# Kernel optimization log

Hardware: AMD Instinct MI355X
Metric: run time of the kernel (lower is better)

The kernel has to match this reference:

```python
import jax, jax.numpy as jnp
import numpy as np

DIMS = 512
B, H, W = 16, 64, 64
C8, C2 = DIMS // 8, DIMS // 2


def _maxpool2(x):
    # 2x2 max pool, stride 2. x: [B, C, H, W] -> [B, C, H//2, W//2]
    b, c, h, w = x.shape
    return x.reshape(b, c, h // 2, 2, w // 2, 2).max(axis=(3, 5))


def _conv1x1(x, w, b):
    # 1x1 conv == channel matmul. x: [B, C_in, H, W], w: [C_out, C_in], b: [C_out]
    return jnp.einsum('oc,bchw->bohw', w, x) + b[None, :, None, None]


def setup_inputs() -> dict:
    key = jax.random.key(0)
    ks = jax.random.split(key, 10)
    s_in = 1.0 / np.sqrt(DIMS)
    s_c2 = 1.0 / np.sqrt(C2)
    return {
        'inputs':  jax.random.normal(ks[0], (B, DIMS, H, W), jnp.float32),
        'w_theta': jax.random.normal(ks[1], (C8, DIMS), jnp.float32) * s_in,
        'b_theta': jax.random.normal(ks[2], (C8,), jnp.float32) * 0.01,
        'w_phi':   jax.random.normal(ks[3], (C8, DIMS), jnp.float32) * s_in,
        'b_phi':   jax.random.normal(ks[4], (C8,), jnp.float32) * 0.01,
        'w_g':     jax.random.normal(ks[5], (C2, DIMS), jnp.float32) * s_in,
        'b_g':     jax.random.normal(ks[6], (C2,), jnp.float32) * 0.01,
        'w_attn':  jax.random.normal(ks[7], (DIMS, C2), jnp.float32) * s_c2,
        'b_attn':  jax.random.normal(ks[8], (DIMS,), jnp.float32) * 0.01,
        'sigma':   jnp.full((1,), 0.5, jnp.float32),
    }


def reference(inputs, w_theta, b_theta, w_phi, b_phi, w_g, b_g, w_attn, b_attn, sigma):
    b, c, h, w = inputs.shape
    hw, hw4 = h * w, (h * w) // 4

    # theta: [B, HW, C//8]
    theta = _conv1x1(inputs, w_theta, b_theta).reshape(b, c // 8, hw).transpose(0, 2, 1)
    # phi: maxpooled keys [B, C//8, HW/4]
    phi = _maxpool2(_conv1x1(inputs, w_phi, b_phi)).reshape(b, c // 8, hw4)
    # attention over downsampled positions
    attn = jax.nn.softmax(jnp.einsum('bnc,bcm->bnm', theta, phi), axis=-1)
    # g: maxpooled values [B, HW/4, C//2]
    g = _maxpool2(_conv1x1(inputs, w_g, b_g)).reshape(b, c // 2, hw4).transpose(0, 2, 1)
    # attend, back to image layout [B, C//2, H, W]
    attn_g = jnp.einsum('bnm,bmc->bnc', attn, g).transpose(0, 2, 1).reshape(b, c // 2, h, w)
    attn_g = _conv1x1(attn_g, w_attn, b_attn)
    return inputs + sigma * attn_g
```

## Files before the change

kernel.cpp:

```cpp
#include <hip/hip_runtime.h>
#include <cstdint>
#include <cstddef>


typedef float f32x4 __attribute__((ext_vector_type(4)));
typedef short bf16x8 __attribute__((ext_vector_type(8)));

static __device__ __forceinline__ float max4f(float a, float b, float c, float d) {
  return fmaxf(fmaxf(a, b), fmaxf(c, d));
}

static __device__ __forceinline__ unsigned short f2bf(float f) {
  unsigned int u = __float_as_uint(f);
  unsigned int r = u + 0x7fffu + ((u >> 16) & 1u);
  return (unsigned short)(r >> 16);
}

__global__ __launch_bounds__(256) void pack_kernel(
    const float* __restrict__ wt, const float* __restrict__ bt,
    const float* __restrict__ wp, const float* __restrict__ bp,
    const float* __restrict__ wg, const float* __restrict__ bg,
    const float* __restrict__ wa,
    unsigned short* __restrict__ Wcat_bf, float* __restrict__ bcat,
    unsigned short* __restrict__ Wa_bf) {
  int i = blockIdx.x * 256 + threadIdx.x;
  if (i < 384 * 512) {
    int o = i >> 9, k = i & 511;
    float v;
    if (o < 64)       v = wt[o * 512 + k];
    else if (o < 128) v = wp[(o - 64) * 512 + k];
    else              v = wg[(o - 128) * 512 + k];
    Wcat_bf[i] = f2bf(v);
  }
  if (i < 512 * 256) Wa_bf[i] = f2bf(wa[i]);
  if (i < 384) {
    float v;
    if (i < 64)       v = bt[i];
    else if (i < 128) v = bp[i - 64];
    else              v = bg[i - 128];
    bcat[i] = v;
  }
}

__global__ __launch_bounds__(256) void transpose_kernel(
    const float* __restrict__ X, unsigned short* __restrict__ Xbf_T) {
  __shared__ unsigned short smT[64 * 516];
  const int b = blockIdx.y, n0 = blockIdx.x * 64;
  const int t = threadIdx.x;
  const float* Xb = X + (size_t)b * 512 * 4096;

  {
    const int nq = t & 15, kr = t >> 4;
#pragma unroll 4
    for (int it = 0; it < 32; ++it) {
      int k = it * 16 + kr;
      float4 v = *(const float4*)&Xb[(size_t)k * 4096 + n0 + nq * 4];
      smT[(nq * 4 + 0) * 516 + k] = f2bf(v.x);
      smT[(nq * 4 + 1) * 516 + k] = f2bf(v.y);
      smT[(nq * 4 + 2) * 516 + k] = f2bf(v.z);
      smT[(nq * 4 + 3) * 516 + k] = f2bf(v.w);
    }
  }
  __syncthreads();

  {
    const int c = t & 63, w = t >> 6;
#pragma unroll 4
    for (int i = 0; i < 16; ++i) {
      int n = w + 4 * i;
      const unsigned short* src = &smT[n * 516 + c * 8];
      uint2 lo = *(const uint2*)&src[0];
      uint2 hi = *(const uint2*)&src[4];
      uint4 v; v.x = lo.x; v.y = lo.y; v.z = hi.x; v.w = hi.y;
      *(uint4*)&Xbf_T[((size_t)b * 4096 + n0 + n) * 512 + c * 8] = v;
    }
  }
}

__global__ __launch_bounds__(256, 3) void conv_pool_kernel(
    const unsigned short* __restrict__ Xbf_T, const unsigned short* __restrict__ Wcat_bf,
    const float* __restrict__ bcat,
    unsigned short* __restrict__ theta_t, unsigned short* __restrict__ phi_t,
    unsigned short* __restrict__ g_t) {
  const int b = blockIdx.z, mt = blockIdx.y, nt = blockIdx.x;
  const int n0 = nt * 128;
  __shared__ float cs[64][132];
  const int t = threadIdx.x;
  const int wave = t >> 6, lane = t & 63;
  const int wm = wave >> 1, wn = wave & 1;
  const int l16 = lane & 15, quad = lane >> 4;

  const unsigned short* aptr =
      Wcat_bf + (size_t)(mt * 128 + wm * 64 + l16) * 512 + quad * 8;
  const unsigned short* bptr =
      Xbf_T + ((size_t)b * 4096 + n0 + wn * 64 + l16) * 512 + quad * 8;

  f32x4 acc[4][4];
#pragma unroll
  for (int i = 0; i < 4; ++i)
#pragma unroll
    for (int j = 0; j < 4; ++j) acc[i][j] = (f32x4)(0.f);

  for (int k0 = 0; k0 < 512; k0 += 32) {
    bf16x8 af[4], bfr[4];
#pragma unroll
    for (int am = 0; am < 4; ++am) af[am] = *(const bf16x8*)(aptr + (size_t)am * 16 * 512 + k0);
#pragma unroll
    for (int bn = 0; bn < 4; ++bn) bfr[bn] = *(const bf16x8*)(bptr + (size_t)bn * 16 * 512 + k0);
#pragma unroll
    for (int am = 0; am < 4; ++am)
#pragma unroll
      for (int bn = 0; bn < 4; ++bn)
        acc[am][bn] = __builtin_amdgcn_mfma_f32_16x16x32_bf16(af[am], bfr[bn], acc[am][bn], 0, 0, 0);
  }

  for (int s = 0; s < 2; ++s) {
    const int m0 = mt * 128 + s * 64;
    const float bias_base = 0.f; (void)bias_base;
    if (wm == s) {
#pragma unroll
      for (int am = 0; am < 4; ++am)
#pragma unroll
        for (int bn = 0; bn < 4; ++bn)
#pragma unroll
          for (int reg = 0; reg < 4; ++reg)
            cs[am * 16 + quad * 4 + reg][wn * 64 + bn * 16 + l16] =
                acc[am][bn][reg] + bcat[m0 + am * 16 + quad * 4 + reg];
    }
    __syncthreads();
    if (m0 < 64) {
      int col = t >> 1, half = t & 1;
      unsigned short vals[32];
#pragma unroll
      for (int i = 0; i < 32; ++i) vals[i] = f2bf(cs[half * 32 + i][col]);
      unsigned short* dst = theta_t + ((size_t)b * 4096 + n0 + col) * 64 + half * 32;
#pragma unroll
      for (int j = 0; j < 4; ++j) ((uint4*)dst)[j] = ((const uint4*)vals)[j];
    } else if (m0 < 128) {
      int px = t >> 3, ch0 = (t & 7) * 8;
      unsigned short v[8];
#pragma unroll
      for (int j = 0; j < 8; ++j) {
        int ch = ch0 + j;
        v[j] = f2bf(max4f(cs[ch][2 * px], cs[ch][2 * px + 1],
                          cs[ch][64 + 2 * px], cs[ch][64 + 2 * px + 1]));
      }
      *(uint4*)&phi_t[((size_t)b * 1024 + nt * 32 + px) * 64 + ch0] = *(const uint4*)v;
    } else {
      int ch = t >> 2, px0 = (t & 3) * 8;
      int gc = m0 - 128 + ch;
      unsigned short v[8];
#pragma unroll
      for (int j = 0; j < 8; ++j) {
        int px = px0 + j;
        v[j] = f2bf(max4f(cs[ch][2 * px], cs[ch][2 * px + 1],
                          cs[ch][64 + 2 * px], cs[ch][64 + 2 * px + 1]));
      }
      *(uint4*)&g_t[((size_t)b * 256 + gc) * 1024 + nt * 32 + px0] = *(const uint4*)v;
    }
    __syncthreads();
  }
}

__global__ __launch_bounds__(256, 2) void attn_kernel(
    const unsigned short* __restrict__ theta, const unsigned short* __restrict__ phi,
    const unsigned short* __restrict__ g, unsigned short* __restrict__ Obf) {
  const int b = blockIdx.y, q0 = blockIdx.x * 32;
  __shared__ unsigned short S_s[32][1032];
  __shared__ float smax[4][32];
  __shared__ float ssum[4][32];
  const int t = threadIdx.x;
  const int w = t >> 6, lane = t & 63;
  const int l16 = lane & 15, quad = lane >> 4;
  const int m0w = w * 256;

  bf16x8 afrag[2][2];
#pragma unroll
  for (int qt = 0; qt < 2; ++qt)
#pragma unroll
    for (int kh = 0; kh < 2; ++kh)
      afrag[qt][kh] = *(const bf16x8*)&theta[((size_t)b * 4096 + q0 + qt * 16 + l16) * 64 +
                                             kh * 32 + quad * 8];

  f32x4 acc[2][16];
#pragma unroll
  for (int qt = 0; qt < 2; ++qt)
#pragma unroll
    for (int mt = 0; mt < 16; ++mt) acc[qt][mt] = (f32x4)(0.f);

  const unsigned short* phiB = phi + (size_t)b * 1024 * 64;
#pragma unroll
  for (int mt = 0; mt < 16; ++mt) {
    int m = m0w + mt * 16 + l16;
    bf16x8 b0 = *(const bf16x8*)&phiB[(size_t)m * 64 + quad * 8];
    bf16x8 b1 = *(const bf16x8*)&phiB[(size_t)m * 64 + 32 + quad * 8];
#pragma unroll
    for (int qt = 0; qt < 2; ++qt) {
      acc[qt][mt] = __builtin_amdgcn_mfma_f32_16x16x32_bf16(afrag[qt][0], b0, acc[qt][mt], 0, 0, 0);
      acc[qt][mt] = __builtin_amdgcn_mfma_f32_16x16x32_bf16(afrag[qt][1], b1, acc[qt][mt], 0, 0, 0);
    }
  }

  float mx8[8];
#pragma unroll
  for (int r = 0; r < 8; ++r) {
    int qt = r >> 2, reg = r & 3;
    float m = acc[qt][0][reg];
#pragma unroll
    for (int mt = 1; mt < 16; ++mt) m = fmaxf(m, acc[qt][mt][reg]);
#pragma unroll
    for (int d = 1; d < 16; d <<= 1) m = fmaxf(m, __shfl_xor(m, d));
    mx8[r] = m;
  }
  if (l16 == 0) {
#pragma unroll
    for (int r = 0; r < 8; ++r) smax[w][(r >> 2) * 16 + quad * 4 + (r & 3)] = mx8[r];
  }
  __syncthreads();
  float gmx[8];
#pragma unroll
  for (int r = 0; r < 8; ++r) {
    int q = (r >> 2) * 16 + quad * 4 + (r & 3);
    gmx[r] = fmaxf(fmaxf(smax[0][q], smax[1][q]), fmaxf(smax[2][q], smax[3][q]));
  }
  float sum8[8];
#pragma unroll
  for (int r = 0; r < 8; ++r) sum8[r] = 0.f;
#pragma unroll
  for (int qt = 0; qt < 2; ++qt)
#pragma unroll
    for (int mt = 0; mt < 16; ++mt)
#pragma unroll
      for (int reg = 0; reg < 4; ++reg) {
        int r = qt * 4 + reg;
        float p = __expf(acc[qt][mt][reg] - gmx[r]);
        acc[qt][mt][reg] = p;
        sum8[r] += p;
      }
#pragma unroll
  for (int r = 0; r < 8; ++r) {
#pragma unroll
    for (int d = 1; d < 16; d <<= 1) sum8[r] += __shfl_xor(sum8[r], d);
  }
  if (l16 == 0) {
#pragma unroll
    for (int r = 0; r < 8; ++r) ssum[w][(r >> 2) * 16 + quad * 4 + (r & 3)] = sum8[r];
  }
  __syncthreads();
  float inv8[8];
#pragma unroll
  for (int r = 0; r < 8; ++r) {
    int q = (r >> 2) * 16 + quad * 4 + (r & 3);
    inv8[r] = 1.0f / (ssum[0][q] + ssum[1][q] + ssum[2][q] + ssum[3][q]);
  }
#pragma unroll
  for (int qt = 0; qt < 2; ++qt)
#pragma unroll
    for (int mt = 0; mt < 16; ++mt)
#pragma unroll
      for (int reg = 0; reg < 4; ++reg) {
        int q = qt * 16 + quad * 4 + reg;
        S_s[q][m0w + mt * 16 + l16] = f2bf(acc[qt][mt][reg] * inv8[qt * 4 + reg]);
      }
  __syncthreads();

  const int cbase = w * 64;
  f32x4 accO[2][4];
#pragma unroll
  for (int qt = 0; qt < 2; ++qt)
#pragma unroll
    for (int ct = 0; ct < 4; ++ct) accO[qt][ct] = (f32x4)(0.f);
  const unsigned short* gB = g + (size_t)b * 256 * 1024;
  for (int k0 = 0; k0 < 1024; k0 += 32) {
    bf16x8 a0 = *(const bf16x8*)&S_s[l16][k0 + quad * 8];
    bf16x8 a1 = *(const bf16x8*)&S_s[16 + l16][k0 + quad * 8];
#pragma unroll
    for (int ct = 0; ct < 4; ++ct) {
      bf16x8 bb = *(const bf16x8*)&gB[(size_t)(cbase + ct * 16 + l16) * 1024 + k0 + quad * 8];
      accO[0][ct] = __builtin_amdgcn_mfma_f32_16x16x32_bf16(a0, bb, accO[0][ct], 0, 0, 0);
      accO[1][ct] = __builtin_amdgcn_mfma_f32_16x16x32_bf16(a1, bb, accO[1][ct], 0, 0, 0);
    }
  }
  unsigned short* Ob = Obf + ((size_t)b * 4096 + q0) * 256;
#pragma unroll
  for (int qt = 0; qt < 2; ++qt)
#pragma unroll
    for (int ct = 0; ct < 4; ++ct)
#pragma unroll
      for (int reg = 0; reg < 4; ++reg)
        Ob[(size_t)(qt * 16 + quad * 4 + reg) * 256 + cbase + ct * 16 + l16] =
            f2bf(accO[qt][ct][reg]);
}

__global__ __launch_bounds__(256, 3) void out_kernel(
    const float* __restrict__ X, const unsigned short* __restrict__ Obf,
    const unsigned short* __restrict__ Wa_bf, const float* __restrict__ ba,
    const float* __restrict__ sigma, float* __restrict__ out) {
  const int b = blockIdx.z, mt = blockIdx.y, nt = blockIdx.x;
  const int t = threadIdx.x;
  const int wave = t >> 6, lane = t & 63;
  const int wm = wave >> 1, wn = wave & 1;
  const int l16 = lane & 15, quad = lane >> 4;

  const unsigned short* aptr = Wa_bf + (size_t)(mt * 128 + wm * 64 + l16) * 256 + quad * 8;
  const unsigned short* bptr =
      Obf + ((size_t)b * 4096 + nt * 128 + wn * 64 + l16) * 256 + quad * 8;

  f32x4 acc[4][4];
#pragma unroll
  for (int i = 0; i < 4; ++i)
#pragma unroll
    for (int j = 0; j < 4; ++j) acc[i][j] = (f32x4)(0.f);

#pragma unroll
  for (int k0 = 0; k0 < 256; k0 += 32) {
    bf16x8 af[4], bfr[4];
#pragma unroll
    for (int am = 0; am < 4; ++am) af[am] = *(const bf16x8*)(aptr + (size_t)am * 16 * 256 + k0);
#pragma unroll
    for (int bn = 0; bn < 4; ++bn) bfr[bn] = *(const bf16x8*)(bptr + (size_t)bn * 16 * 256 + k0);
#pragma unroll
    for (int am = 0; am < 4; ++am)
#pragma unroll
      for (int bn = 0; bn < 4; ++bn)
        acc[am][bn] = __builtin_amdgcn_mfma_f32_16x16x32_bf16(af[am], bfr[bn], acc[am][bn], 0, 0, 0);
  }

  const float sg = sigma[0];
#pragma unroll
  for (int am = 0; am < 4; ++am) {
#pragma unroll
    for (int reg = 0; reg < 4; ++reg) {
      int m = mt * 128 + wm * 64 + am * 16 + quad * 4 + reg;
      float bias = ba[m];
      size_t rowoff = ((size_t)b * 512 + m) * 4096 + nt * 128 + wn * 64;
#pragma unroll
      for (int bn = 0; bn < 4; ++bn) {
        size_t idx = rowoff + bn * 16 + l16;
        out[idx] = X[idx] + sg * (acc[am][bn][reg] + bias);
      }
    }
  }
}

extern "C" void kernel_launch(void* const* d_in, const int* in_sizes, int n_in,
                              void* d_out, int out_size, void* d_ws, size_t ws_size,
                              hipStream_t stream) {
  (void)in_sizes; (void)n_in; (void)out_size; (void)ws_size;
  const float* X  = (const float*)d_in[0];
  const float* wt = (const float*)d_in[1];
  const float* bt = (const float*)d_in[2];
  const float* wp = (const float*)d_in[3];
  const float* bp = (const float*)d_in[4];
  const float* wg = (const float*)d_in[5];
  const float* bg = (const float*)d_in[6];
  const float* wa = (const float*)d_in[7];
  const float* ba = (const float*)d_in[8];
  const float* sg = (const float*)d_in[9];
  float* out = (float*)d_out;
  char* base = (char*)d_ws;

  unsigned short* Wcat_bf = (unsigned short*)(base);
  unsigned short* Wa_bf   = (unsigned short*)(base + 0x60000);
  float*          bcat    = (float*)(base + 0xA0000);
  unsigned short* theta_t = (unsigned short*)(base + (1u << 20));
  unsigned short* phi_t   = (unsigned short*)(base + (9u << 20));
  unsigned short* g_t     = (unsigned short*)(base + (11u << 20));
  unsigned short* Xbf_T   = (unsigned short*)(base + (19u << 20));
  unsigned short* Obf     = (unsigned short*)(base + (19u << 20));

  pack_kernel<<<dim3(768), dim3(256), 0, stream>>>(wt, bt, wp, bp, wg, bg, wa,
                                                   Wcat_bf, bcat, Wa_bf);
  transpose_kernel<<<dim3(64, 16), dim3(256), 0, stream>>>(X, Xbf_T);
  conv_pool_kernel<<<dim3(32, 3, 16), dim3(256), 0, stream>>>(Xbf_T, Wcat_bf, bcat,
                                                              theta_t, phi_t, g_t);
  attn_kernel<<<dim3(128, 16), dim3(256), 0, stream>>>(theta_t, phi_t, g_t, Obf);
  out_kernel<<<dim3(32, 4, 16), dim3(256), 0, stream>>>(X, Obf, Wa_bf, ba, sg, out);
}
```

Measured before the change: 607.2 us.

## Stage GEMM tiles via async global-to-LDS loads and widen attention to 8 waves

The conv_pool and out GEMM kernels now stage each 32-wide K slice of both operands into LDS with global_load_lds 16-byte async copies. The MFMA fragments are then read from LDS instead of being loaded directly from global memory by each wave, which aims to cut redundant global traffic and improve coalescing. The price is two barriers per K step and no double buffering, so load latency is not overlapped with compute. Separately, attn_kernel moves to 512 threads (8 waves), each wave covering half as many keys and output channels. Its softmax now combines per-wave max and sum statistics in one pass, removing a barrier.

Result: faster. 573.9 us (-5.5%).

```diff
diff --git a/kernel.cpp b/kernel.cpp
--- a/kernel.cpp
+++ b/kernel.cpp
@@ -14,6 +14,12 @@
   unsigned int u = __float_as_uint(f);
   unsigned int r = u + 0x7fffu + ((u >> 16) & 1u);
   return (unsigned short)(r >> 16);
+}
+
+static __device__ __forceinline__ void async_ld16(void* lds, const void* g) {
+  __builtin_amdgcn_global_load_lds(
+      (const __attribute__((address_space(1))) unsigned int*)g,
+      (__attribute__((address_space(3))) unsigned int*)lds, 16, 0, 0);
 }
 
 __global__ __launch_bounds__(256) void pack_kernel(
@@ -62,7 +68,6 @@
     }
   }
   __syncthreads();
-
   {
     const int c = t & 63, w = t >> 6;
 #pragma unroll 4
@@ -84,16 +89,19 @@
     unsigned short* __restrict__ g_t) {
   const int b = blockIdx.z, mt = blockIdx.y, nt = blockIdx.x;
   const int n0 = nt * 128;
-  __shared__ float cs[64][132];
+  __shared__ union {
+    struct { unsigned short A[128 * 32]; unsigned short B[128 * 32]; } st;
+    float cs[64][132];
+  } sm;
   const int t = threadIdx.x;
   const int wave = t >> 6, lane = t & 63;
   const int wm = wave >> 1, wn = wave & 1;
   const int l16 = lane & 15, quad = lane >> 4;
-
-  const unsigned short* aptr =
-      Wcat_bf + (size_t)(mt * 128 + wm * 64 + l16) * 512 + quad * 8;
-  const unsigned short* bptr =
-      Xbf_T + ((size_t)b * 4096 + n0 + wn * 64 + l16) * 512 + quad * 8;
+  const int srow = lane >> 2, skq = (lane & 3) * 8;
+
+  const unsigned short* gA = Wcat_bf + (size_t)(mt * 128) * 512 + skq;
+  const unsigned short* gB = Xbf_T + ((size_t)b * 4096 + n0) * 512 + skq;
+  const int r0 = wave * 32;
 
   f32x4 acc[4][4];
 #pragma unroll
@@ -101,22 +109,31 @@
 #pragma unroll
     for (int j = 0; j < 4; ++j) acc[i][j] = (f32x4)(0.f);
 
+  const int abase = (wm * 64 + l16) * 32 + quad * 8;
+  const int bbase = (wn * 64 + l16) * 32 + quad * 8;
+
   for (int k0 = 0; k0 < 512; k0 += 32) {
+    __syncthreads();
+    async_ld16(&sm.st.A[(r0) * 32],      gA + (size_t)(r0 + srow) * 512 + k0);
+    async_ld16(&sm.st.A[(r0 + 16) * 32], gA + (size_t)(r0 + 16 + srow) * 512 + k0);
+    async_ld16(&sm.st.B[(r0) * 32],      gB + (size_t)(r0 + srow) * 512 + k0);
+    async_ld16(&sm.st.B[(r0 + 16) * 32], gB + (size_t)(r0 + 16 + srow) * 512 + k0);
+    __syncthreads();
     bf16x8 af[4], bfr[4];
 #pragma unroll
-    for (int am = 0; am < 4; ++am) af[am] = *(const bf16x8*)(aptr + (size_t)am * 16 * 512 + k0);
-#pragma unroll
-    for (int bn = 0; bn < 4; ++bn) bfr[bn] = *(const bf16x8*)(bptr + (size_t)bn * 16 * 512 + k0);
+    for (int am = 0; am < 4; ++am) af[am] = *(const bf16x8*)&sm.st.A[abase + am * 16 * 32];
+#pragma unroll
+    for (int bn = 0; bn < 4; ++bn) bfr[bn] = *(const bf16x8*)&sm.st.B[bbase + bn * 16 * 32];
 #pragma unroll
     for (int am = 0; am < 4; ++am)
 #pragma unroll
       for (int bn = 0; bn < 4; ++bn)
         acc[am][bn] = __builtin_amdgcn_mfma_f32_16x16x32_bf16(af[am], bfr[bn], acc[am][bn], 0, 0, 0);
   }
+  __syncthreads();
 
   for (int s = 0; s < 2; ++s) {
     const int m0 = mt * 128 + s * 64;
-    const float bias_base = 0.f; (void)bias_base;
     if (wm == s) {
 #pragma unroll
       for (int am = 0; am < 4; ++am)
@@ -124,7 +141,7 @@
         for (int bn = 0; bn < 4; ++bn)
 #pragma unroll
           for (int reg = 0; reg < 4; ++reg)
-            cs[am * 16 + quad * 4 + reg][wn * 64 + bn * 16 + l16] =
+            sm.cs[am * 16 + quad * 4 + reg][wn * 64 + bn * 16 + l16] =
                 acc[am][bn][reg] + bcat[m0 + am * 16 + quad * 4 + reg];
     }
     __syncthreads();
@@ -132,7 +149,7 @@
       int col = t >> 1, half = t & 1;
       unsigned short vals[32];
 #pragma unroll
-      for (int i = 0; i < 32; ++i) vals[i] = f2bf(cs[half * 32 + i][col]);
+      for (int i = 0; i < 32; ++i) vals[i] = f2bf(sm.cs[half * 32 + i][col]);
       unsigned short* dst = theta_t + ((size_t)b * 4096 + n0 + col) * 64 + half * 32;
 #pragma unroll
       for (int j = 0; j < 4; ++j) ((uint4*)dst)[j] = ((const uint4*)vals)[j];
@@ -142,8 +159,8 @@
 #pragma unroll
       for (int j = 0; j < 8; ++j) {
         int ch = ch0 + j;
-        v[j] = f2bf(max4f(cs[ch][2 * px], cs[ch][2 * px + 1],
-                          cs[ch][64 + 2 * px], cs[ch][64 + 2 * px + 1]));
+        v[j] = f2bf(max4f(sm.cs[ch][2 * px], sm.cs[ch][2 * px + 1],
+                          sm.cs[ch][64 + 2 * px], sm.cs[ch][64 + 2 * px + 1]));
       }
       *(uint4*)&phi_t[((size_t)b * 1024 + nt * 32 + px) * 64 + ch0] = *(const uint4*)v;
     } else {
@@ -153,8 +170,8 @@
 #pragma unroll
       for (int j = 0; j < 8; ++j) {
         int px = px0 + j;
-        v[j] = f2bf(max4f(cs[ch][2 * px], cs[ch][2 * px + 1],
-                          cs[ch][64 + 2 * px], cs[ch][64 + 2 * px + 1]));
+        v[j] = f2bf(max4f(sm.cs[ch][2 * px], sm.cs[ch][2 * px + 1],
+                          sm.cs[ch][64 + 2 * px], sm.cs[ch][64 + 2 * px + 1]));
       }
       *(uint4*)&g_t[((size_t)b * 256 + gc) * 1024 + nt * 32 + px0] = *(const uint4*)v;
     }
@@ -162,17 +179,16 @@
   }
 }
 
-__global__ __launch_bounds__(256, 2) void attn_kernel(
+__global__ __launch_bounds__(512, 4) void attn_kernel(
     const unsigned short* __restrict__ theta, const unsigned short* __restrict__ phi,
     const unsigned short* __restrict__ g, unsigned short* __restrict__ Obf) {
   const int b = blockIdx.y, q0 = blockIdx.x * 32;
   __shared__ unsigned short S_s[32][1032];
-  __shared__ float smax[4][32];
-  __shared__ float ssum[4][32];
+  __shared__ float2 sstat[32][8];
   const int t = threadIdx.x;
   const int w = t >> 6, lane = t & 63;
   const int l16 = lane & 15, quad = lane >> 4;
-  const int m0w = w * 256;
+  const int m0w = w * 128;
 
   bf16x8 afrag[2][2];
 #pragma unroll
@@ -182,15 +198,15 @@
       afrag[qt][kh] = *(const bf16x8*)&theta[((size_t)b * 4096 + q0 + qt * 16 + l16) * 64 +
                                              kh * 32 + quad * 8];
 
-  f32x4 acc[2][16];
-#pragma unroll
-  for (int qt = 0; qt < 2; ++qt)
-#pragma unroll
-    for (int mt = 0; mt < 16; ++mt) acc[qt][mt] = (f32x4)(0.f);
+  f32x4 acc[2][8];
+#pragma unroll
+  for (int qt = 0; qt < 2; ++qt)
+#pragma unroll
+    for (int mt = 0; mt < 8; ++mt) acc[qt][mt] = (f32x4)(0.f);
 
   const unsigned short* phiB = phi + (size_t)b * 1024 * 64;
 #pragma unroll
-  for (int mt = 0; mt < 16; ++mt) {
+  for (int mt = 0; mt < 8; ++mt) {
     int m = m0w + mt * 16 + l16;
     bf16x8 b0 = *(const bf16x8*)&phiB[(size_t)m * 64 + quad * 8];
     bf16x8 b1 = *(const bf16x8*)&phiB[(size_t)m * 64 + 32 + quad * 8];
@@ -201,39 +217,26 @@
     }
   }
 
-  float mx8[8];
+  float mx8[8], sum8[8];
 #pragma unroll
   for (int r = 0; r < 8; ++r) {
     int qt = r >> 2, reg = r & 3;
     float m = acc[qt][0][reg];
 #pragma unroll
-    for (int mt = 1; mt < 16; ++mt) m = fmaxf(m, acc[qt][mt][reg]);
+    for (int mt = 1; mt < 8; ++mt) m = fmaxf(m, acc[qt][mt][reg]);
 #pragma unroll
     for (int d = 1; d < 16; d <<= 1) m = fmaxf(m, __shfl_xor(m, d));
     mx8[r] = m;
-  }
-  if (l16 == 0) {
-#pragma unroll
-    for (int r = 0; r < 8; ++r) smax[w][(r >> 2) * 16 + quad * 4 + (r & 3)] = mx8[r];
-  }
-  __syncthreads();
-  float gmx[8];
-#pragma unroll
-  for (int r = 0; r < 8; ++r) {
-    int q = (r >> 2) * 16 + quad * 4 + (r & 3);
-    gmx[r] = fmaxf(fmaxf(smax[0][q], smax[1][q]), fmaxf(smax[2][q], smax[3][q]));
-  }
-  float sum8[8];
-#pragma unroll
-  for (int r = 0; r < 8; ++r) sum8[r] = 0.f;
-#pragma unroll
-  for (int qt = 0; qt < 2; ++qt)
-#pragma unroll
-    for (int mt = 0; mt < 16; ++mt)
+    sum8[r] = 0.f;
+  }
+#pragma unroll
+  for (int qt = 0; qt < 2; ++qt)
+#pragma unroll
+    for (int mt = 0; mt < 8; ++mt)
 #pragma unroll
       for (int reg = 0; reg < 4; ++reg) {
         int r = qt * 4 + reg;
-        float p = __expf(acc[qt][mt][reg] - gmx[r]);
+        float p = __expf(acc[qt][mt][reg] - mx8[r]);
         acc[qt][mt][reg] = p;
         sum8[r] += p;
       }
@@ -244,38 +247,51 @@
   }
   if (l16 == 0) {
 #pragma unroll
-    for (int r = 0; r < 8; ++r) ssum[w][(r >> 2) * 16 + quad * 4 + (r & 3)] = sum8[r];
+    for (int r = 0; r < 8; ++r) {
+      int q = (r >> 2) * 16 + quad * 4 + (r & 3);
+      sstat[q][w] = make_float2(mx8[r], sum8[r]);
+    }
   }
   __syncthreads();
-  float inv8[8];
+
+  float alpha[8];
 #pragma unroll
   for (int r = 0; r < 8; ++r) {
     int q = (r >> 2) * 16 + quad * 4 + (r & 3);
-    inv8[r] = 1.0f / (ssum[0][q] + ssum[1][q] + ssum[2][q] + ssum[3][q]);
-  }
-#pragma unroll
-  for (int qt = 0; qt < 2; ++qt)
-#pragma unroll
-    for (int mt = 0; mt < 16; ++mt)
+    float2 st[8];
+#pragma unroll
+    for (int j = 0; j < 4; ++j) ((float4*)st)[j] = *(const float4*)&sstat[q][j * 2];
+    float mg = st[0].x;
+#pragma unroll
+    for (int j = 1; j < 8; ++j) mg = fmaxf(mg, st[j].x);
+    float sg = 0.f;
+#pragma unroll
+    for (int j = 0; j < 8; ++j) sg += st[j].y * __expf(st[j].x - mg);
+    alpha[r] = __expf(mx8[r] - mg) / sg;
+  }
+#pragma unroll
+  for (int qt = 0; qt < 2; ++qt)
+#pragma unroll
+    for (int mt = 0; mt < 8; ++mt)
 #pragma unroll
       for (int reg = 0; reg < 4; ++reg) {
         int q = qt * 16 + quad * 4 + reg;
-        S_s[q][m0w + mt * 16 + l16] = f2bf(acc[qt][mt][reg] * inv8[qt * 4 + reg]);
+        S_s[q][m0w + mt * 16 + l16] = f2bf(acc[qt][mt][reg] * alpha[qt * 4 + reg]);
       }
   __syncthreads();
 
-  const int cbase = w * 64;
-  f32x4 accO[2][4];
-#pragma unroll
-  for (int qt = 0; qt < 2; ++qt)
-#pragma unroll
-    for (int ct = 0; ct < 4; ++ct) accO[qt][ct] = (f32x4)(0.f);
+  const int cbase = w * 32;
+  f32x4 accO[2][2];
+#pragma unroll
+  for (int qt = 0; qt < 2; ++qt)
+#pragma unroll
+    for (int ct = 0; ct < 2; ++ct) accO[qt][ct] = (f32x4)(0.f);
   const unsigned short* gB = g + (size_t)b * 256 * 1024;
   for (int k0 = 0; k0 < 1024; k0 += 32) {
     bf16x8 a0 = *(const bf16x8*)&S_s[l16][k0 + quad * 8];
     bf16x8 a1 = *(const bf16x8*)&S_s[16 + l16][k0 + quad * 8];
 #pragma unroll
-    for (int ct = 0; ct < 4; ++ct) {
+    for (int ct = 0; ct < 2; ++ct) {
       bf16x8 bb = *(const bf16x8*)&gB[(size_t)(cbase + ct * 16 + l16) * 1024 + k0 + quad * 8];
       accO[0][ct] = __builtin_amdgcn_mfma_f32_16x16x32_bf16(a0, bb, accO[0][ct], 0, 0, 0);
       accO[1][ct] = __builtin_amdgcn_mfma_f32_16x16x32_bf16(a1, bb, accO[1][ct], 0, 0, 0);
@@ -285,7 +301,7 @@
 #pragma unroll
   for (int qt = 0; qt < 2; ++qt)
 #pragma unroll
-    for (int ct = 0; ct < 4; ++ct)
+    for (int ct = 0; ct < 2; ++ct)
 #pragma unroll
       for (int reg = 0; reg < 4; ++reg)
         Ob[(size_t)(qt * 16 + quad * 4 + reg) * 256 + cbase + ct * 16 + l16] =
@@ -297,14 +313,16 @@
     const unsigned short* __restrict__ Wa_bf, const float* __restrict__ ba,
     const float* __restrict__ sigma, float* __restrict__ out) {
   const int b = blockIdx.z, mt = blockIdx.y, nt = blockIdx.x;
+  __shared__ struct { unsigned short A[128 * 32]; unsigned short B[128 * 32]; } sm;
   const int t = threadIdx.x;
   const int wave = t >> 6, lane = t & 63;
   const int wm = wave >> 1, wn = wave & 1;
   const int l16 = lane & 15, quad = lane >> 4;
-
-  const unsigned short* aptr = Wa_bf + (size_t)(mt * 128 + wm * 64 + l16) * 256 + quad * 8;
-  const unsigned short* bptr =
-      Obf + ((size_t)b * 4096 + nt * 128 + wn * 64 + l16) * 256 + quad * 8;
+  const int srow = lane >> 2, skq = (lane & 3) * 8;
+
+  const unsigned short* gA = Wa_bf + (size_t)(mt * 128) * 256 + skq;
+  const unsigned short* gB = Obf + ((size_t)b * 4096 + nt * 128) * 256 + skq;
+  const int r0 = wave * 32;
 
   f32x4 acc[4][4];
 #pragma unroll
@@ -312,13 +330,21 @@
 #pragma unroll
     for (int j = 0; j < 4; ++j) acc[i][j] = (f32x4)(0.f);
 
-#pragma unroll
+  const int abase = (wm * 64 + l16) * 32 + quad * 8;
+  const int bbase = (wn * 64 + l16) * 32 + quad * 8;
+
   for (int k0 = 0; k0 < 256; k0 += 32) {
+    __syncthreads();
+    async_ld16(&sm.A[(r0) * 32],      gA + (size_t)(r0 + srow) * 256 + k0);
+    async_ld16(&sm.A[(r0 + 16) * 32], gA + (size_t)(r0 + 16 + srow) * 256 + k0);
+    async_ld16(&sm.B[(r0) * 32],      gB + (size_t)(r0 + srow) * 256 + k0);
+    async_ld16(&sm.B[(r0 + 16) * 32], gB + (size_t)(r0 + 16 + srow) * 256 + k0);
+    __syncthreads();
     bf16x8 af[4], bfr[4];
 #pragma unroll
-    for (int am = 0; am < 4; ++am) af[am] = *(const bf16x8*)(aptr + (size_t)am * 16 * 256 + k0);
-#pragma unroll
-    for (int bn = 0; bn < 4; ++bn) bfr[bn] = *(const bf16x8*)(bptr + (size_t)bn * 16 * 256 + k0);
+    for (int am = 0; am < 4; ++am) af[am] = *(const bf16x8*)&sm.A[abase + am * 16 * 32];
+#pragma unroll
+    for (int bn = 0; bn < 4; ++bn) bfr[bn] = *(const bf16x8*)&sm.B[bbase + bn * 16 * 32];
 #pragma unroll
     for (int am = 0; am < 4; ++am)
 #pragma unroll
@@ -374,6 +400,6 @@
   transpose_kernel<<<dim3(64, 16), dim3(256), 0, stream>>>(X, Xbf_T);
   conv_pool_kernel<<<dim3(32, 3, 16), dim3(256), 0, stream>>>(Xbf_T, Wcat_bf, bcat,
                                                               theta_t, phi_t, g_t);
-  attn_kernel<<<dim3(128, 16), dim3(256), 0, stream>>>(theta_t, phi_t, g_t, Obf);
+  attn_kernel<<<dim3(128, 16), dim3(512), 0, stream>>>(theta_t, phi_t, g_t, Obf);
   out_kernel<<<dim3(32, 4, 16), dim3(256), 0, stream>>>(X, Obf, Wa_bf, ba, sg, out);
 }
```
